# Kernel optimization log

Measured on AMD Instinct MI355X. Metric: run time of the kernel, lower is better.

## Reference

```python
import jax, jax.numpy as jnp
import numpy as np


def setup_inputs() -> dict:
    key = jax.random.key(0)
    k1, k2, k3, k4, k5 = jax.random.split(key, 5)
    B, Cin, D, H, W = 16, 16, 32, 32, 32
    Cout, Kd = 32, 3
    return {
        "x": jax.random.normal(k1, (B, Cin, D, H, W), dtype=jnp.float32),
        "weight": jax.random.normal(k2, (Cout, Cin, Kd, Kd, Kd), dtype=jnp.float32),
        "conv_bias": jax.random.normal(k3, (Cout,), dtype=jnp.float32),
        "scaling_factor": jax.random.normal(k4, (Cout, 1, 1, 1), dtype=jnp.float32),
        "bias_param": jax.random.normal(k5, (Cout, 1, 1, 1), dtype=jnp.float32),
    }


def reference(x, weight, conv_bias, scaling_factor, bias_param):
    # 3D valid conv, stride 1, NCDHW layout / OIDHW kernel
    y = jax.lax.conv_general_dilated(
        x, weight,
        window_strides=(1, 1, 1),
        padding="VALID",
        dimension_numbers=("NCDHW", "OIDHW", "NCDHW"),
    )
    # per-channel bias, scale, tanh, scale, sigmoid (broadcast over D,H,W)
    y = y + conv_bias[None, :, None, None, None]
    y = jnp.tanh(y * scaling_factor[None]) * bias_param[None]
    return jax.nn.sigmoid(y)
```

## Files before the change

### kernel.cpp

```cpp
#include <hip/hip_runtime.h>

#define NB    16
#define CIN   16
#define COUT  32
#define DIN   32
#define DOUT  30

typedef __attribute__((ext_vector_type(8)))  short  short8;
typedef __attribute__((ext_vector_type(16))) float  f32x16;

static __device__ __forceinline__ unsigned short f2bf_rne(float f) {
    unsigned int u = __builtin_bit_cast(unsigned int, f);
    u += 0x7fffu + ((u >> 16) & 1u);
    return (unsigned short)(u >> 16);
}
static __device__ __forceinline__ float bf2f(unsigned short s) {
    unsigned int u = ((unsigned int)s) << 16;
    return __builtin_bit_cast(float, u);
}

__global__ __launch_bounds__(64) void repack_w(const float* __restrict__ wgt,
                                               short* __restrict__ ws) {
    const int s  = blockIdx.x;
    const int l  = threadIdx.x;
    const int co  = l & 31;
    const int ci0 = (l >> 5) * 8;
    short8 vh, vl;
#pragma unroll
    for (int j = 0; j < 8; ++j) {
        float f = wgt[co * (CIN * 27) + (ci0 + j) * 27 + s];
        unsigned short h = f2bf_rne(f);
        vh[j] = (short)h;
        vl[j] = (short)f2bf_rne(f - bf2f(h));
    }
    ((short8*)ws)[s * 64 + l]            = vh;
    ((short8*)ws)[27 * 64 + s * 64 + l]  = vl;
}

__global__ __launch_bounds__(256) void conv3d_mfma(
    const float* __restrict__ x,
    const short* __restrict__ wsA,
    const float* __restrict__ cbias,
    const float* __restrict__ scal,
    const float* __restrict__ bpar,
    float* __restrict__ out)
{
    __shared__ short sx[2 * 9216];
    __shared__ float sp[96];

    const int htile = blockIdx.x;
    const int d     = blockIdx.y;
    const int b     = blockIdx.z;

    const int tid  = threadIdx.x;
    const int wy   = tid >> 6;
    const int lane = tid & 63;

    if (tid < 32) {
        sp[tid]      = cbias[tid];
        sp[32 + tid] = scal[tid];
        sp[64 + tid] = bpar[tid];
    }

    const int h0 = htile * 4;

    const int xb = b * (CIN * DIN * DIN * DIN);
    for (int c = tid; c < 1152; c += 256) {
        const int hi8 = c & 1;
        const int r2  = c >> 1;
        const int w   = r2 & 31;
        const int rr  = r2 >> 5;
        const int dz  = rr / 6;
        const int row = rr - dz * 6;
        int h_in = h0 + row; if (h_in > 31) h_in = 31;
        const int gbase = xb + (hi8 * 8) * (DIN * DIN * DIN)
                        + (d + dz) * (DIN * DIN) + h_in * DIN + w;
        short8 vh, vl;
#pragma unroll
        for (int j = 0; j < 8; ++j) {
            float f = x[gbase + j * (DIN * DIN * DIN)];
            unsigned short h = f2bf_rne(f);
            vh[j] = (short)h;
            vl[j] = (short)f2bf_rne(f - bf2f(h));
        }
        *(short8*)(sx + c * 8)        = vh;
        *(short8*)(sx + 9216 + c * 8) = vl;
    }
    __syncthreads();

    const int h = h0 + wy;
    if (h >= DOUT) return;

    const int n  = lane & 31;
    const int hi = lane >> 5;

    int wofs[3];
#pragma unroll
    for (int kw = 0; kw < 3; ++kw) {
        int wc = n + kw; if (wc > 31) wc = 31;
        wofs[kw] = wc * 16 + hi * 8;
    }

    f32x16 acc;
#pragma unroll
    for (int i = 0; i < 16; ++i) acc[i] = 0.0f;

    const short8* wa = (const short8*)wsA;
#pragma unroll
    for (int kd = 0; kd < 3; ++kd) {
#pragma unroll
        for (int kh = 0; kh < 3; ++kh) {
            const int rbase = (kd * 6 + wy + kh) * (32 * 16);
#pragma unroll
            for (int kw = 0; kw < 3; ++kw) {
                const int s = kd * 9 + kh * 3 + kw;
                short8 ah = wa[s * 64 + lane];
                short8 al = wa[1728 + s * 64 + lane];
                short8 bh = *(const short8*)(sx + rbase + wofs[kw]);
                short8 bl = *(const short8*)(sx + 9216 + rbase + wofs[kw]);
                acc = __builtin_amdgcn_mfma_f32_32x32x16_bf16(ah, bh, acc, 0, 0, 0);
                acc = __builtin_amdgcn_mfma_f32_32x32x16_bf16(ah, bl, acc, 0, 0, 0);
                acc = __builtin_amdgcn_mfma_f32_32x32x16_bf16(al, bh, acc, 0, 0, 0);
            }
        }
    }

    if (n < DOUT) {
        const int obase = b * (COUT * DOUT * DOUT * DOUT)
                        + d * (DOUT * DOUT) + h * DOUT + n;
#pragma unroll
        for (int r = 0; r < 16; ++r) {
            const int co = (r & 3) + 8 * (r >> 2) + 4 * hi;
            float y  = acc[r] + sp[co];
            float t  = y * sp[32 + co];
            float th = 1.0f - 2.0f / (__expf(2.0f * t) + 1.0f);
            float z  = th * sp[64 + co];
            float rr = 1.0f / (1.0f + __expf(-z));
            out[obase + co * (DOUT * DOUT * DOUT)] = rr;
        }
    }
}

extern "C" void kernel_launch(void* const* d_in, const int* in_sizes, int n_in,
                              void* d_out, int out_size, void* d_ws, size_t ws_size,
                              hipStream_t stream) {
    const float* x     = (const float*)d_in[0];
    const float* wgt   = (const float*)d_in[1];
    const float* cbias = (const float*)d_in[2];
    const float* scal  = (const float*)d_in[3];
    const float* bpar  = (const float*)d_in[4];
    float* out = (float*)d_out;
    short* ws  = (short*)d_ws;

    hipLaunchKernelGGL(repack_w, dim3(27), dim3(64), 0, stream, wgt, ws);
    hipLaunchKernelGGL(conv3d_mfma, dim3(8, DOUT, NB), dim3(256), 0, stream,
                       x, ws, cbias, scal, bpar, out);
}
```

Measured before the change: 147.1 us.

## Process two output depth slices per block and reorganize LDS layout

Each block now computes two adjacent output depth slices with 8 waves, sharing a 4-deep input halo in LDS instead of loading 3 slices per single output slice. This cuts redundant global loads and bf16 split conversions. The LDS layout moves the channel-half bit above w, which changes the bank pattern of the B-operand reads. The split conversion now uses the packed v_cvt_pk_bf16_f32 instruction. Block size doubles and LDS use grows, which may lower occupancy.

```diff
diff --git a/kernel.cpp b/kernel.cpp
--- a/kernel.cpp
+++ b/kernel.cpp
@@ -6,8 +6,9 @@
 #define DIN   32
 #define DOUT  30
 
-typedef __attribute__((ext_vector_type(8)))  short  short8;
-typedef __attribute__((ext_vector_type(16))) float  f32x16;
+typedef __attribute__((ext_vector_type(8)))  short        short8;
+typedef __attribute__((ext_vector_type(4)))  unsigned int uint4v;
+typedef __attribute__((ext_vector_type(16))) float        f32x16;
 
 static __device__ __forceinline__ unsigned short f2bf_rne(float f) {
     unsigned int u = __builtin_bit_cast(unsigned int, f);
@@ -17,6 +18,11 @@
 static __device__ __forceinline__ float bf2f(unsigned short s) {
     unsigned int u = ((unsigned int)s) << 16;
     return __builtin_bit_cast(float, u);
+}
+static __device__ __forceinline__ unsigned int cvt_pk_bf16(float a, float b) {
+    unsigned int r;
+    asm("v_cvt_pk_bf16_f32 %0, %1, %2" : "=v"(r) : "v"(a), "v"(b));
+    return r;
 }
 
 __global__ __launch_bounds__(64) void repack_w(const float* __restrict__ wgt,
@@ -37,7 +43,7 @@
     ((short8*)ws)[27 * 64 + s * 64 + l]  = vl;
 }
 
-__global__ __launch_bounds__(256) void conv3d_mfma(
+__global__ __launch_bounds__(512) void conv3d_mfma(
     const float* __restrict__ x,
     const short* __restrict__ wsA,
     const float* __restrict__ cbias,
@@ -45,15 +51,17 @@
     const float* __restrict__ bpar,
     float* __restrict__ out)
 {
-    __shared__ short sx[2 * 9216];
+    __shared__ __align__(16) short sx[2 * 12288];
     __shared__ float sp[96];
 
     const int htile = blockIdx.x;
-    const int d     = blockIdx.y;
+    const int dpair = blockIdx.y;
     const int b     = blockIdx.z;
 
     const int tid  = threadIdx.x;
-    const int wy   = tid >> 6;
+    const int ww   = tid >> 6;
+    const int wd   = ww >> 2;
+    const int wy   = ww & 3;
     const int lane = tid & 63;
 
     if (tid < 32) {
@@ -63,33 +71,40 @@
     }
 
     const int h0 = htile * 4;
+    const int d0 = dpair * 2;
 
     const int xb = b * (CIN * DIN * DIN * DIN);
-    for (int c = tid; c < 1152; c += 256) {
-        const int hi8 = c & 1;
-        const int r2  = c >> 1;
-        const int w   = r2 & 31;
-        const int rr  = r2 >> 5;
+    for (int c = tid; c < 1536; c += 512) {
+        const int w   = c & 31;
+        const int hi8 = (c >> 5) & 1;
+        const int rr  = c >> 6;
         const int dz  = rr / 6;
         const int row = rr - dz * 6;
         int h_in = h0 + row; if (h_in > 31) h_in = 31;
         const int gbase = xb + (hi8 * 8) * (DIN * DIN * DIN)
-                        + (d + dz) * (DIN * DIN) + h_in * DIN + w;
-        short8 vh, vl;
+                        + (d0 + dz) * (DIN * DIN) + h_in * DIN + w;
+        float f[8];
 #pragma unroll
-        for (int j = 0; j < 8; ++j) {
-            float f = x[gbase + j * (DIN * DIN * DIN)];
-            unsigned short h = f2bf_rne(f);
-            vh[j] = (short)h;
-            vl[j] = (short)f2bf_rne(f - bf2f(h));
+        for (int j = 0; j < 8; ++j) f[j] = x[gbase + j * (DIN * DIN * DIN)];
+        uint4v vh, vl;
+#pragma unroll
+        for (int j = 0; j < 8; j += 2) {
+            unsigned int hp = cvt_pk_bf16(f[j], f[j + 1]);
+            float b0 = __builtin_bit_cast(float, hp << 16);
+            float b1 = __builtin_bit_cast(float, hp & 0xffff0000u);
+            unsigned int lp = cvt_pk_bf16(f[j] - b0, f[j + 1] - b1);
+            vh[j >> 1] = hp;
+            vl[j >> 1] = lp;
         }
-        *(short8*)(sx + c * 8)        = vh;
-        *(short8*)(sx + 9216 + c * 8) = vl;
+        const int idx = rr * 64 + hi8 * 32 + w;
+        *(uint4v*)(sx + idx * 8)             = vh;
+        *(uint4v*)(sx + 12288 + idx * 8)     = vl;
     }
     __syncthreads();
 
     const int h = h0 + wy;
     if (h >= DOUT) return;
+    const int d = d0 + wd;
 
     const int n  = lane & 31;
     const int hi = lane >> 5;
@@ -98,7 +113,7 @@
 #pragma unroll
     for (int kw = 0; kw < 3; ++kw) {
         int wc = n + kw; if (wc > 31) wc = 31;
-        wofs[kw] = wc * 16 + hi * 8;
+        wofs[kw] = hi * 256 + wc * 8;
     }
 
     f32x16 acc;
@@ -110,14 +125,14 @@
     for (int kd = 0; kd < 3; ++kd) {
 #pragma unroll
         for (int kh = 0; kh < 3; ++kh) {
-            const int rbase = (kd * 6 + wy + kh) * (32 * 16);
+            const int rbase = ((wd + kd) * 6 + wy + kh) * 512;
 #pragma unroll
             for (int kw = 0; kw < 3; ++kw) {
                 const int s = kd * 9 + kh * 3 + kw;
                 short8 ah = wa[s * 64 + lane];
                 short8 al = wa[1728 + s * 64 + lane];
                 short8 bh = *(const short8*)(sx + rbase + wofs[kw]);
-                short8 bl = *(const short8*)(sx + 9216 + rbase + wofs[kw]);
+                short8 bl = *(const short8*)(sx + 12288 + rbase + wofs[kw]);
                 acc = __builtin_amdgcn_mfma_f32_32x32x16_bf16(ah, bh, acc, 0, 0, 0);
                 acc = __builtin_amdgcn_mfma_f32_32x32x16_bf16(ah, bl, acc, 0, 0, 0);
                 acc = __builtin_amdgcn_mfma_f32_32x32x16_bf16(al, bh, acc, 0, 0, 0);
@@ -153,6 +168,6 @@
     short* ws  = (short*)d_ws;
 
     hipLaunchKernelGGL(repack_w, dim3(27), dim3(64), 0, stream, wgt, ws);
-    hipLaunchKernelGGL(conv3d_mfma, dim3(8, DOUT, NB), dim3(256), 0, stream,
+    hipLaunchKernelGGL(conv3d_mfma, dim3(8, 15, NB), dim3(512), 0, stream,
                        x, ws, cbias, scal, bpar, out);
 }
```

New measurement: 147.6 us. Within noise of the previous version (+0.4%).
